# Optimization experiments

Measured on AMD Instinct MI355X. Metric: run time of the kernel, lower is better.

The kernel has to match this reference:

```python
import jax, jax.numpy as jnp
jax.config.update("jax_enable_x64", True)
import numpy as np

B, S, D, H = 2, 1024, 1024, 16
DEPTH = D // H  # 64


def setup_inputs() -> dict:
    key = jax.random.key(0)
    ks = jax.random.split(key, 12)
    inp = {
        "q": jax.random.normal(ks[0], (B, S, D), jnp.float32),
        "k": jax.random.normal(ks[1], (B, S, D), jnp.float32),
        "v": jax.random.normal(ks[2], (B, S - 1, D), jnp.float32),
        "e": jnp.zeros((1,), jnp.float32),  # unused by the layer
        "mask": jax.random.randint(ks[3], (B, S - 1, S - 1), 0, 2, jnp.int32),
        "Wq": jax.random.normal(ks[4], (D, D), jnp.float32) * 0.02,
        "bq": jnp.zeros((D,), jnp.float32),
        "Wk": jax.random.normal(ks[5], (D, D), jnp.float32) * 0.02,
        "bk": jnp.zeros((D,), jnp.float32),
        "Wv": jax.random.normal(ks[6], (D, D), jnp.float32) * 0.02,
        "bv": jnp.zeros((D,), jnp.float32),
        "Wo": jax.random.normal(ks[7], (D, D), jnp.float32) * 0.02,
        "bo": jnp.zeros((D,), jnp.float32),
    }
    return inp


def _split_heads(x, b):
    # [b, s, D] -> [b, H, s, DEPTH]
    return x.reshape(b, -1, H, DEPTH).transpose(0, 2, 1, 3)


def reference(q, k, v, e, mask, Wq, bq, Wk, bk, Wv, bv, Wo, bo):
    b = q.shape[0]
    qh = _split_heads(q @ Wq + bq, b)  # [b,H,S,dh]
    kh = _split_heads(k @ Wk + bk, b)  # [b,H,S,dh]
    vh = _split_heads(v @ Wv + bv, b)  # [b,H,S-1,dh]
    # QK^T then asymmetric offset slice [1:, :-1]
    scores = jnp.einsum("bhqd,bhkd->bhqk", qh, kh)[:, :, 1:, :-1]  # [b,H,S-1,S-1]
    inv_sqrt_dk = 1.0 / jnp.sqrt(jnp.float32(DEPTH))
    nl_qk = jax.nn.relu(scores * inv_sqrt_dk).astype(jnp.float64)
    nl_qk = nl_qk + mask[:, None, :, :].astype(jnp.float64) * (-1e9)
    att_weights = jax.nn.softmax(nl_qk, axis=-1)  # fp64, [b,H,S-1,S-1]
    out = jnp.einsum("bhqk,bhkd->bhqd", att_weights, vh.astype(jnp.float64))
    out = out.transpose(0, 2, 1, 3).reshape(b, -1, H * DEPTH)  # [b,S-1,D]
    output = out.astype(jnp.float32) @ Wo + bo
    return (output, att_weights)
```

## Files before the change

kernel.cpp:

```cpp
#include <hip/hip_runtime.h>
#include <math.h>

#define HN 16
#define SEQ 1024
#define DMODEL 1024
#define DH 64
#define SM1 1023

typedef float  f32x4  __attribute__((ext_vector_type(4)));
typedef __bf16 bf16x8 __attribute__((ext_vector_type(8)));

template<int MODE>
__global__ __launch_bounds__(256)
void gemm_mfma_kernel(const float* __restrict__ X, const float* __restrict__ W,
                      const float* __restrict__ bias, float* __restrict__ out32,
                      __bf16* __restrict__ outHi, __bf16* __restrict__ outLo,
                      int M, int rows)
{
    __shared__ __align__(16) __bf16 As[4096];
    __shared__ __align__(16) __bf16 Bs[4096];

    const int t  = threadIdx.x;
    const int w  = t >> 6, l = t & 63;
    const int lr = l & 15, ls = l >> 4;
    const int m0 = blockIdx.y * 64, n0 = blockIdx.x * 64;
    const int sr  = t >> 2;
    const int skq = t & 3;

    f32x4 acc[4];
#pragma unroll
    for (int ct = 0; ct < 4; ++ct) acc[ct] = f32x4{0.f, 0.f, 0.f, 0.f};

    const int ar   = w * 16 + lr;
    const int a_hi = ar * 128 + (((2 * ls    ) ^ (ar & 7)) << 4);
    const int a_lo = ar * 128 + (((2 * ls + 1) ^ (ar & 7)) << 4);
    const int st_hi = sr * 128 + (((2 * skq    ) ^ (sr & 7)) << 4);
    const int st_lo = sr * 128 + (((2 * skq + 1) ^ (sr & 7)) << 4);

    for (int k0 = 0; k0 < DMODEL; k0 += 32) {
        __syncthreads();
        {
            float xv[8];
            if (m0 + sr < M) {
                float4 v0 = *(const float4*)&X[(size_t)(m0 + sr) * DMODEL + k0 + skq * 8];
                float4 v1 = *(const float4*)&X[(size_t)(m0 + sr) * DMODEL + k0 + skq * 8 + 4];
                xv[0] = v0.x; xv[1] = v0.y; xv[2] = v0.z; xv[3] = v0.w;
                xv[4] = v1.x; xv[5] = v1.y; xv[6] = v1.z; xv[7] = v1.w;
            } else {
#pragma unroll
                for (int e = 0; e < 8; ++e) xv[e] = 0.f;
            }
            bf16x8 h8, l8;
#pragma unroll
            for (int e = 0; e < 8; ++e) {
                __bf16 hb = (__bf16)xv[e];
                h8[e] = hb;
                l8[e] = (__bf16)(xv[e] - (float)hb);
            }
            *(bf16x8*)((char*)As + st_hi) = h8;
            *(bf16x8*)((char*)As + st_lo) = l8;
        }
        {
            float wv[8];
#pragma unroll
            for (int e = 0; e < 8; ++e)
                wv[e] = W[(size_t)(k0 + skq * 8 + e) * DMODEL + n0 + sr];
            bf16x8 h8, l8;
#pragma unroll
            for (int e = 0; e < 8; ++e) {
                __bf16 hb = (__bf16)wv[e];
                h8[e] = hb;
                l8[e] = (__bf16)(wv[e] - (float)hb);
            }
            *(bf16x8*)((char*)Bs + st_hi) = h8;
            *(bf16x8*)((char*)Bs + st_lo) = l8;
        }
        __syncthreads();

        const bf16x8 ah = *(const bf16x8*)((const char*)As + a_hi);
        const bf16x8 al = *(const bf16x8*)((const char*)As + a_lo);
#pragma unroll
        for (int ct = 0; ct < 4; ++ct) {
            const int bc   = ct * 16 + lr;
            const int b_hi = bc * 128 + (((2 * ls    ) ^ (bc & 7)) << 4);
            const int b_lo = bc * 128 + (((2 * ls + 1) ^ (bc & 7)) << 4);
            const bf16x8 bh = *(const bf16x8*)((const char*)Bs + b_hi);
            const bf16x8 bl = *(const bf16x8*)((const char*)Bs + b_lo);
            acc[ct] = __builtin_amdgcn_mfma_f32_16x16x32_bf16(ah, bh, acc[ct], 0, 0, 0);
            acc[ct] = __builtin_amdgcn_mfma_f32_16x16x32_bf16(al, bh, acc[ct], 0, 0, 0);
            acc[ct] = __builtin_amdgcn_mfma_f32_16x16x32_bf16(ah, bl, acc[ct], 0, 0, 0);
        }
    }

#pragma unroll
    for (int ct = 0; ct < 4; ++ct) {
        const int n = n0 + ct * 16 + lr;
        const float bv = bias[n];
#pragma unroll
        for (int j = 0; j < 4; ++j) {
            const int m = m0 + w * 16 + ls * 4 + j;
            if (m >= M) continue;
            const float val = acc[ct][j] + bv;
            if (MODE == 1) {
                out32[(size_t)m * DMODEL + n] = val;
            } else {
                const int bb = m / rows, s = m - bb * rows;
                const __bf16 hb = (__bf16)val;
                const __bf16 lb = (__bf16)(val - (float)hb);
                size_t idx;
                if (MODE == 0)
                    idx = (((size_t)(bb * HN + (n >> 6)) * SEQ + s) << 6) + (n & 63);
                else
                    idx = (((size_t)(bb * HN + (n >> 6)) * DH + (n & 63)) << 10) + s;
                outHi[idx] = hb; outLo[idx] = lb;
            }
        }
    }
}

__global__ __launch_bounds__(256)
void mask_pack_kernel(const int* __restrict__ mask, unsigned int* __restrict__ mb)
{
    const int row = blockIdx.x * 4 + (threadIdx.x >> 6);
    const int l   = threadIdx.x & 63;
    if (row >= 2 * SM1) return;
    const int* mrow = mask + (size_t)row * SM1;
    unsigned int* out = mb + (size_t)row * 32;
#pragma unroll
    for (int i = 0; i < 16; ++i) {
        const int c = i * 64 + l;
        const bool mv = (c < SM1) && (mrow[c] != 0);
        unsigned long long bal = __ballot(mv);
        if (l == 0) {
            out[i * 2]     = (unsigned int)bal;
            out[i * 2 + 1] = (unsigned int)(bal >> 32);
        }
    }
}

__global__ __launch_bounds__(512, 4)
void attn_fused_kernel(const __bf16* __restrict__ qhi, const __bf16* __restrict__ qlo,
                       const __bf16* __restrict__ khi, const __bf16* __restrict__ klo,
                       const __bf16* __restrict__ vthi, const __bf16* __restrict__ vtlo,
                       const unsigned int* __restrict__ mbG,
                       float* __restrict__ att, float* __restrict__ ctx)
{
    __shared__ __align__(16) char QE[64 * 528];
    __shared__ __align__(16) char KV[32768];
    __shared__ unsigned int mbitsT[32][64];
    __shared__ float invs[64];
    __shared__ float partial[64][2];

    const int id  = blockIdx.x;
    const int xcd = id & 7, slot = id >> 3;
    const int bh  = xcd + 8 * (slot >> 4);
    const int b   = bh >> 4, h = bh & 15;
    const int q0  = (slot & 15) * 64;

    const int t = threadIdx.x, w = t >> 6, l = t & 63;
    const int lr = l & 15, ls = l >> 4;
    const int g = w & 3, p = w >> 2;

#pragma unroll
    for (int it = 0; it < 2; ++it) {
        const int idq = t + it * 512;
        const int r = idq >> 4, cw = idq & 15;
        const int plane = cw >> 3, s = cw & 7;
        int qrow = q0 + r + 1; if (qrow > 1023) qrow = 1023;
        const __bf16* src = plane ? qlo : qhi;
        bf16x8 vv = *(const bf16x8*)&src[((size_t)bh * SEQ + qrow) * DH + s * 8];
        *(bf16x8*)(QE + r * 256 + ((cw ^ (r & 15)) << 4)) = vv;
    }
#pragma unroll
    for (int it = 0; it < 4; ++it) {
        const int idm = t + it * 512;
        const int cw = idm & 31, r = idm >> 5;
        const int rr = q0 + r;
        mbitsT[cw][r] = (rr < SM1) ? mbG[((size_t)b * SM1 + rr) * 32 + cw] : 0u;
    }
    __syncthreads();

    const int ar = g * 16 + lr;
    const bf16x8 a0h = *(const bf16x8*)(QE + ar * 256 + (((ls     ) ^ lr) << 4));
    const bf16x8 a1h = *(const bf16x8*)(QE + ar * 256 + ((( 4 + ls) ^ lr) << 4));
    const bf16x8 a0l = *(const bf16x8*)(QE + ar * 256 + ((( 8 + ls) ^ lr) << 4));
    const bf16x8 a1l = *(const bf16x8*)(QE + ar * 256 + (((12 + ls) ^ lr) << 4));
    __syncthreads();

    float rsum[4] = {0.f, 0.f, 0.f, 0.f};
    for (int kt = 0; kt < 8; ++kt) {
        const int c0 = kt * 128;
        __syncthreads();
#pragma unroll
        for (int it = 0; it < 4; ++it) {
            const int idk = t + it * 512;
            const int r = idk >> 4, cw = idk & 15;
            const int plane = cw >> 3, s = cw & 7;
            int krow = c0 + r; if (krow > 1023) krow = 1023;
            const __bf16* src = plane ? klo : khi;
            bf16x8 vv = *(const bf16x8*)&src[((size_t)bh * SEQ + krow) * DH + s * 8];
            *(bf16x8*)(KV + r * 256 + ((cw ^ (r & 15)) << 4)) = vv;
        }
        __syncthreads();

#pragma unroll
        for (int i = 0; i < 4; ++i) {
            const int ct = p * 4 + i;
            const int kr = ct * 16 + lr;
            const bf16x8 b0h = *(const bf16x8*)(KV + kr * 256 + (((ls     ) ^ lr) << 4));
            const bf16x8 b1h = *(const bf16x8*)(KV + kr * 256 + ((( 4 + ls) ^ lr) << 4));
            const bf16x8 b0l = *(const bf16x8*)(KV + kr * 256 + ((( 8 + ls) ^ lr) << 4));
            const bf16x8 b1l = *(const bf16x8*)(KV + kr * 256 + (((12 + ls) ^ lr) << 4));

            f32x4 acc = {0.f, 0.f, 0.f, 0.f};
            __builtin_amdgcn_s_setprio(1);
            acc = __builtin_amdgcn_mfma_f32_16x16x32_bf16(a0h, b0h, acc, 0, 0, 0);
            acc = __builtin_amdgcn_mfma_f32_16x16x32_bf16(a0l, b0h, acc, 0, 0, 0);
            acc = __builtin_amdgcn_mfma_f32_16x16x32_bf16(a0h, b0l, acc, 0, 0, 0);
            acc = __builtin_amdgcn_mfma_f32_16x16x32_bf16(a1h, b1h, acc, 0, 0, 0);
            acc = __builtin_amdgcn_mfma_f32_16x16x32_bf16(a1l, b1h, acc, 0, 0, 0);
            acc = __builtin_amdgcn_mfma_f32_16x16x32_bf16(a1h, b1l, acc, 0, 0, 0);
            __builtin_amdgcn_s_setprio(0);

            const int c = c0 + ct * 16 + lr;
            const int wmi = kt * 4 + (ct >> 1);
#pragma unroll
            for (int j = 0; j < 4; ++j) {
                const int r = q0 + g * 16 + ls * 4 + j;
                if (r < SM1 && c < SM1) {
                    float sc = fmaxf(acc[j] * 0.125f, 0.f);
                    const unsigned int wm = mbitsT[wmi][g * 16 + ls * 4 + j];
                    if ((wm >> ((ct & 1) * 16 + lr)) & 1u) sc = -1e9f;
                    rsum[j] += __expf(sc);
                }
            }
        }
    }
#pragma unroll
    for (int j = 0; j < 4; ++j) {
        rsum[j] += __shfl_xor(rsum[j], 1, 64);
        rsum[j] += __shfl_xor(rsum[j], 2, 64);
        rsum[j] += __shfl_xor(rsum[j], 4, 64);
        rsum[j] += __shfl_xor(rsum[j], 8, 64);
    }
    if (lr == 0) {
#pragma unroll
        for (int j = 0; j < 4; ++j)
            partial[g * 16 + ls * 4 + j][p] = rsum[j];
    }
    __syncthreads();
    if (t < 64) {
        const float s = partial[t][0] + partial[t][1];
        invs[t] = (q0 + t < SM1) ? 1.0f / s : 0.f;
    }
    __syncthreads();
    float inv4[4];
#pragma unroll
    for (int j = 0; j < 4; ++j) inv4[j] = invs[g * 16 + ls * 4 + j];

    float* E = (float*)QE;
    f32x4 oacc[4];
#pragma unroll
    for (int ct = 0; ct < 4; ++ct) oacc[ct] = f32x4{0.f, 0.f, 0.f, 0.f};

    for (int kt = 0; kt < 8; ++kt) {
        const int c0 = kt * 128;
        __syncthreads();
#pragma unroll
        for (int it = 0; it < 4; ++it) {
            const int idk = t + it * 512;
            const int r = idk >> 4, cw = idk & 15;
            const int plane = cw >> 3, s = cw & 7;
            int krow = c0 + r; if (krow > 1023) krow = 1023;
            const __bf16* src = plane ? klo : khi;
            bf16x8 vv = *(const bf16x8*)&src[((size_t)bh * SEQ + krow) * DH + s * 8];
            *(bf16x8*)(KV + r * 256 + ((cw ^ (r & 15)) << 4)) = vv;
        }
        __syncthreads();

#pragma unroll
        for (int i = 0; i < 4; ++i) {
            const int ct = p * 4 + i;
            const int kr = ct * 16 + lr;
            const bf16x8 b0h = *(const bf16x8*)(KV + kr * 256 + (((ls     ) ^ lr) << 4));
            const bf16x8 b1h = *(const bf16x8*)(KV + kr * 256 + ((( 4 + ls) ^ lr) << 4));
            const bf16x8 b0l = *(const bf16x8*)(KV + kr * 256 + ((( 8 + ls) ^ lr) << 4));
            const bf16x8 b1l = *(const bf16x8*)(KV + kr * 256 + (((12 + ls) ^ lr) << 4));

            f32x4 acc = {0.f, 0.f, 0.f, 0.f};
            __builtin_amdgcn_s_setprio(1);
            acc = __builtin_amdgcn_mfma_f32_16x16x32_bf16(a0h, b0h, acc, 0, 0, 0);
            acc = __builtin_amdgcn_mfma_f32_16x16x32_bf16(a0l, b0h, acc, 0, 0, 0);
            acc = __builtin_amdgcn_mfma_f32_16x16x32_bf16(a0h, b0l, acc, 0, 0, 0);
            acc = __builtin_amdgcn_mfma_f32_16x16x32_bf16(a1h, b1h, acc, 0, 0, 0);
            acc = __builtin_amdgcn_mfma_f32_16x16x32_bf16(a1l, b1h, acc, 0, 0, 0);
            acc = __builtin_amdgcn_mfma_f32_16x16x32_bf16(a1h, b1l, acc, 0, 0, 0);
            __builtin_amdgcn_s_setprio(0);

            const int c = c0 + ct * 16 + lr;
            const int wmi = kt * 4 + (ct >> 1);
#pragma unroll
            for (int j = 0; j < 4; ++j) {
                const int r = q0 + g * 16 + ls * 4 + j;
                float v = 0.f;
                if (r < SM1 && c < SM1) {
                    float sc = fmaxf(acc[j] * 0.125f, 0.f);
                    const unsigned int wm = mbitsT[wmi][g * 16 + ls * 4 + j];
                    if ((wm >> ((ct & 1) * 16 + lr)) & 1u) sc = -1e9f;
                    v = __expf(sc) * inv4[j];
                }
                E[(g * 16 + ls * 4 + j) * 132 + ct * 16 + lr] = v;
            }
        }
        __syncthreads();

#pragma unroll
        for (int it = 0; it < 4; ++it) {
            const int idv = t + it * 512;
            const int dr = idv >> 5, cw = idv & 31;
            const int plane = cw >> 4, s8 = cw & 15;
            const __bf16* src = plane ? vtlo : vthi;
            bf16x8 vv = *(const bf16x8*)&src[(((size_t)bh * DH + dr) << 10) + c0 + s8 * 8];
            *(bf16x8*)(KV + dr * 512 + ((cw ^ (dr & 31)) << 4)) = vv;
        }
#pragma unroll
        for (int it = 0; it < 4; ++it) {
            const int idw = t + it * 512;
            const int r = idw >> 5, q4 = idw & 31;
            const int rr = q0 + r, cc = c0 + q4 * 4;
            if (rr < SM1) {
                f32x4 vv = *(const f32x4*)&E[r * 132 + q4 * 4];
                float* dst = &att[((size_t)bh * SM1 + rr) * SM1 + cc];
                if (cc + 4 <= SM1) {
                    __builtin_nontemporal_store(vv, (f32x4*)dst);
                } else {
                    if (cc + 0 < SM1) dst[0] = vv.x;
                    if (cc + 1 < SM1) dst[1] = vv.y;
                    if (cc + 2 < SM1) dst[2] = vv.z;
                }
            }
        }
        __syncthreads();

#pragma unroll
        for (int m = 0; m < 2; ++m) {
            const int ks = p * 2 + m;
            const int pr = g * 16 + lr;
            const f32x4 p0 = *(const f32x4*)&E[pr * 132 + ks * 32 + ls * 8];
            const f32x4 p1 = *(const f32x4*)&E[pr * 132 + ks * 32 + ls * 8 + 4];
            float pf[8] = {p0.x, p0.y, p0.z, p0.w, p1.x, p1.y, p1.z, p1.w};
            bf16x8 ph, pl;
#pragma unroll
            for (int e = 0; e < 8; ++e) {
                const __bf16 hb = (__bf16)pf[e];
                ph[e] = hb;
                pl[e] = (__bf16)(pf[e] - (float)hb);
            }
#pragma unroll
            for (int ct = 0; ct < 4; ++ct) {
                const int vr = ct * 16 + lr;
                const int hslot = ((ks * 4 + ls) ^ (vr & 31));
                const int lslot = ((16 + ks * 4 + ls) ^ (vr & 31));
                const bf16x8 vh = *(const bf16x8*)(KV + vr * 512 + (hslot << 4));
                const bf16x8 vl = *(const bf16x8*)(KV + vr * 512 + (lslot << 4));
                __builtin_amdgcn_s_setprio(1);
                oacc[ct] = __builtin_amdgcn_mfma_f32_16x16x32_bf16(ph, vh, oacc[ct], 0, 0, 0);
                oacc[ct] = __builtin_amdgcn_mfma_f32_16x16x32_bf16(pl, vh, oacc[ct], 0, 0, 0);
                oacc[ct] = __builtin_amdgcn_mfma_f32_16x16x32_bf16(ph, vl, oacc[ct], 0, 0, 0);
                __builtin_amdgcn_s_setprio(0);
            }
        }
    }

    __syncthreads();
    float* red = (float*)QE;
    if (p == 1) {
#pragma unroll
        for (int ct = 0; ct < 4; ++ct)
#pragma unroll
            for (int j = 0; j < 4; ++j)
                red[(g * 16 + ls * 4 + j) * 68 + ct * 16 + lr] = oacc[ct][j];
    }
    __syncthreads();
    if (p == 0) {
#pragma unroll
        for (int ct = 0; ct < 4; ++ct)
#pragma unroll
            for (int j = 0; j < 4; ++j) {
                const int r = q0 + g * 16 + ls * 4 + j;
                if (r < SM1)
                    ctx[((size_t)b * SM1 + r) * DMODEL + h * DH + ct * 16 + lr] =
                        oacc[ct][j] + red[(g * 16 + ls * 4 + j) * 68 + ct * 16 + lr];
            }
    }
}

extern "C" void kernel_launch(void* const* d_in, const int* in_sizes, int n_in,
                              void* d_out, int out_size, void* d_ws, size_t ws_size,
                              hipStream_t stream) {
    const float* q    = (const float*)d_in[0];
    const float* k    = (const float*)d_in[1];
    const float* v    = (const float*)d_in[2];
    const int*   mask = (const int*)  d_in[4];
    const float* Wq   = (const float*)d_in[5];
    const float* bq   = (const float*)d_in[6];
    const float* Wk   = (const float*)d_in[7];
    const float* bk   = (const float*)d_in[8];
    const float* Wv   = (const float*)d_in[9];
    const float* bv   = (const float*)d_in[10];
    const float* Wo   = (const float*)d_in[11];
    const float* bo   = (const float*)d_in[12];

    float* out0 = (float*)d_out;
    float* att  = out0 + (size_t)2 * SM1 * DMODEL;

    const size_t NQ  = (size_t)2 * HN * SEQ * DH;
    const size_t NVT = (size_t)2 * HN * DH * 1024;
    __bf16* ws16 = (__bf16*)d_ws;
    __bf16* qhi  = ws16;
    __bf16* qlo  = qhi + NQ;
    __bf16* khi  = qlo + NQ;
    __bf16* klo  = khi + NQ;
    __bf16* vthi = klo + NQ;
    __bf16* vtlo = vthi + NVT;
    float*  ctx  = (float*)(vtlo + NVT);
    unsigned int* mbG = (unsigned int*)(ctx + (size_t)2 * SM1 * DMODEL);

    (void)hipMemsetAsync(vthi, 0, 2 * NVT * sizeof(__bf16), stream);

    mask_pack_kernel<<<dim3(512), 256, 0, stream>>>(mask, mbG);

    gemm_mfma_kernel<0><<<dim3(16, 32), 256, 0, stream>>>(q, Wq, bq, nullptr, qhi, qlo, 2 * SEQ, SEQ);
    gemm_mfma_kernel<0><<<dim3(16, 32), 256, 0, stream>>>(k, Wk, bk, nullptr, khi, klo, 2 * SEQ, SEQ);
    gemm_mfma_kernel<2><<<dim3(16, 32), 256, 0, stream>>>(v, Wv, bv, nullptr, vthi, vtlo, 2 * SM1, SM1);

    attn_fused_kernel<<<dim3(512), 512, 0, stream>>>(qhi, qlo, khi, klo, vthi, vtlo, mbG, att, ctx);

    gemm_mfma_kernel<1><<<dim3(16, 32), 256, 0, stream>>>(ctx, Wo, bo, out0, nullptr, nullptr, 2 * SM1, SM1);
}
```

Baseline: 265.5 us.

## Prefetch GEMM and attention tiles into registers to overlap global loads

The projection GEMM moves to double-buffered shared memory, with the next K-slice loaded into registers during the MFMA work on the current one, so there is one barrier per iteration instead of two. In the attention kernel, the K and V tiles are register-prefetched one step ahead in both passes, and the V load is issued while the score tile is still being computed. The goal is to hide global-memory latency behind MFMA work, at the cost of more registers and more shared memory in the GEMM, which may reduce occupancy.

Measured after the change: 276.3 us. 1.04x slower.

```diff
diff --git a/kernel.cpp b/kernel.cpp
--- a/kernel.cpp
+++ b/kernel.cpp
@@ -17,8 +17,8 @@
                       __bf16* __restrict__ outHi, __bf16* __restrict__ outLo,
                       int M, int rows)
 {
-    __shared__ __align__(16) __bf16 As[4096];
-    __shared__ __align__(16) __bf16 Bs[4096];
+    __shared__ __align__(16) __bf16 As[2][4096];
+    __shared__ __align__(16) __bf16 Bs[2][4096];
 
     const int t  = threadIdx.x;
     const int w  = t >> 6, l = t & 63;
@@ -26,6 +26,7 @@
     const int m0 = blockIdx.y * 64, n0 = blockIdx.x * 64;
     const int sr  = t >> 2;
     const int skq = t & 3;
+    const bool arow_ok = (m0 + sr < M);
 
     f32x4 acc[4];
 #pragma unroll
@@ -37,59 +38,61 @@
     const int st_hi = sr * 128 + (((2 * skq    ) ^ (sr & 7)) << 4);
     const int st_lo = sr * 128 + (((2 * skq + 1) ^ (sr & 7)) << 4);
 
-    for (int k0 = 0; k0 < DMODEL; k0 += 32) {
-        __syncthreads();
-        {
-            float xv[8];
-            if (m0 + sr < M) {
-                float4 v0 = *(const float4*)&X[(size_t)(m0 + sr) * DMODEL + k0 + skq * 8];
-                float4 v1 = *(const float4*)&X[(size_t)(m0 + sr) * DMODEL + k0 + skq * 8 + 4];
-                xv[0] = v0.x; xv[1] = v0.y; xv[2] = v0.z; xv[3] = v0.w;
-                xv[4] = v1.x; xv[5] = v1.y; xv[6] = v1.z; xv[7] = v1.w;
-            } else {
-#pragma unroll
-                for (int e = 0; e < 8; ++e) xv[e] = 0.f;
-            }
-            bf16x8 h8, l8;
-#pragma unroll
-            for (int e = 0; e < 8; ++e) {
-                __bf16 hb = (__bf16)xv[e];
-                h8[e] = hb;
-                l8[e] = (__bf16)(xv[e] - (float)hb);
-            }
-            *(bf16x8*)((char*)As + st_hi) = h8;
-            *(bf16x8*)((char*)As + st_lo) = l8;
-        }
-        {
-            float wv[8];
-#pragma unroll
-            for (int e = 0; e < 8; ++e)
-                wv[e] = W[(size_t)(k0 + skq * 8 + e) * DMODEL + n0 + sr];
-            bf16x8 h8, l8;
-#pragma unroll
-            for (int e = 0; e < 8; ++e) {
-                __bf16 hb = (__bf16)wv[e];
-                h8[e] = hb;
-                l8[e] = (__bf16)(wv[e] - (float)hb);
-            }
-            *(bf16x8*)((char*)Bs + st_hi) = h8;
-            *(bf16x8*)((char*)Bs + st_lo) = l8;
-        }
-        __syncthreads();
-
-        const bf16x8 ah = *(const bf16x8*)((const char*)As + a_hi);
-        const bf16x8 al = *(const bf16x8*)((const char*)As + a_lo);
+    float4 xv0, xv1;
+    float  wv[8];
+
+    auto LOADT = [&](int k0) {
+        if (arow_ok) {
+            xv0 = *(const float4*)&X[(size_t)(m0 + sr) * DMODEL + k0 + skq * 8];
+            xv1 = *(const float4*)&X[(size_t)(m0 + sr) * DMODEL + k0 + skq * 8 + 4];
+        } else {
+            xv0 = float4{0.f, 0.f, 0.f, 0.f};
+            xv1 = float4{0.f, 0.f, 0.f, 0.f};
+        }
+#pragma unroll
+        for (int e = 0; e < 8; ++e)
+            wv[e] = W[(size_t)(k0 + skq * 8 + e) * DMODEL + n0 + sr];
+    };
+    auto WRITET = [&](int buf) {
+        float xa[8] = {xv0.x, xv0.y, xv0.z, xv0.w, xv1.x, xv1.y, xv1.z, xv1.w};
+        bf16x8 ah8, al8, bh8, bl8;
+#pragma unroll
+        for (int e = 0; e < 8; ++e) {
+            __bf16 hb = (__bf16)xa[e];
+            ah8[e] = hb;
+            al8[e] = (__bf16)(xa[e] - (float)hb);
+            __bf16 wb = (__bf16)wv[e];
+            bh8[e] = wb;
+            bl8[e] = (__bf16)(wv[e] - (float)wb);
+        }
+        *(bf16x8*)((char*)As[buf] + st_hi) = ah8;
+        *(bf16x8*)((char*)As[buf] + st_lo) = al8;
+        *(bf16x8*)((char*)Bs[buf] + st_hi) = bh8;
+        *(bf16x8*)((char*)Bs[buf] + st_lo) = bl8;
+    };
+
+    LOADT(0);
+    WRITET(0);
+
+    for (int ks = 0; ks < 32; ++ks) {
+        const int cur = ks & 1;
+        if (ks < 31) LOADT((ks + 1) * 32);
+        __syncthreads();
+
+        const bf16x8 ah = *(const bf16x8*)((const char*)As[cur] + a_hi);
+        const bf16x8 al = *(const bf16x8*)((const char*)As[cur] + a_lo);
 #pragma unroll
         for (int ct = 0; ct < 4; ++ct) {
             const int bc   = ct * 16 + lr;
             const int b_hi = bc * 128 + (((2 * ls    ) ^ (bc & 7)) << 4);
             const int b_lo = bc * 128 + (((2 * ls + 1) ^ (bc & 7)) << 4);
-            const bf16x8 bh = *(const bf16x8*)((const char*)Bs + b_hi);
-            const bf16x8 bl = *(const bf16x8*)((const char*)Bs + b_lo);
+            const bf16x8 bh = *(const bf16x8*)((const char*)Bs[cur] + b_hi);
+            const bf16x8 bl = *(const bf16x8*)((const char*)Bs[cur] + b_lo);
             acc[ct] = __builtin_amdgcn_mfma_f32_16x16x32_bf16(ah, bh, acc[ct], 0, 0, 0);
             acc[ct] = __builtin_amdgcn_mfma_f32_16x16x32_bf16(al, bh, acc[ct], 0, 0, 0);
             acc[ct] = __builtin_amdgcn_mfma_f32_16x16x32_bf16(ah, bl, acc[ct], 0, 0, 0);
         }
+        if (ks < 31) WRITET(cur ^ 1);
     }
 
 #pragma unroll
@@ -161,6 +164,34 @@
     const int lr = l & 15, ls = l >> 4;
     const int g = w & 3, p = w >> 2;
 
+    int k_roff[4], k_doff[4], k_soff[4];
+#pragma unroll
+    for (int it = 0; it < 4; ++it) {
+        const int idk = t + it * 512;
+        const int r = idk >> 4, cw = idk & 15;
+        k_roff[it] = r;
+        k_soff[it] = (cw & 7) * 8 + ((cw >> 3) ? 1 : 0) * 0;
+        k_doff[it] = r * 256 + ((cw ^ (r & 15)) << 4);
+    }
+    int k_plane[4];
+#pragma unroll
+    for (int it = 0; it < 4; ++it) {
+        const int idk = t + it * 512;
+        k_plane[it] = (idk & 15) >> 3;
+    }
+    int v_droff[4], v_soff[4], v_doff[4], v_plane[4];
+#pragma unroll
+    for (int it = 0; it < 4; ++it) {
+        const int idv = t + it * 512;
+        const int dr = idv >> 5, cw = idv & 31;
+        v_droff[it] = dr;
+        v_plane[it] = cw >> 4;
+        v_soff[it]  = (cw & 15) * 8;
+        v_doff[it]  = dr * 512 + ((cw ^ (dr & 31)) << 4);
+    }
+
+    bf16x8 kr[4], vr[4];
+
 #pragma unroll
     for (int it = 0; it < 2; ++it) {
         const int idq = t + it * 512;
@@ -187,30 +218,52 @@
     const bf16x8 a1l = *(const bf16x8*)(QE + ar * 256 + (((12 + ls) ^ lr) << 4));
     __syncthreads();
 
+#define LOADK(c0_)                                                              \
+    {                                                                           \
+        _Pragma("unroll")                                                       \
+        for (int it = 0; it < 4; ++it) {                                        \
+            int krow = (c0_) + k_roff[it]; if (krow > 1023) krow = 1023;        \
+            const __bf16* src = k_plane[it] ? klo : khi;                        \
+            kr[it] = *(const bf16x8*)&src[((size_t)bh * SEQ + krow) * DH + k_soff[it]]; \
+        }                                                                       \
+    }
+#define WRITEK()                                                                \
+    {                                                                           \
+        _Pragma("unroll")                                                       \
+        for (int it = 0; it < 4; ++it)                                          \
+            *(bf16x8*)(KV + k_doff[it]) = kr[it];                               \
+    }
+#define LOADV(c0_)                                                              \
+    {                                                                           \
+        _Pragma("unroll")                                                       \
+        for (int it = 0; it < 4; ++it) {                                        \
+            const __bf16* src = v_plane[it] ? vtlo : vthi;                      \
+            vr[it] = *(const bf16x8*)&src[(((size_t)bh * DH + v_droff[it]) << 10) + (c0_) + v_soff[it]]; \
+        }                                                                       \
+    }
+#define WRITEV()                                                                \
+    {                                                                           \
+        _Pragma("unroll")                                                       \
+        for (int it = 0; it < 4; ++it)                                          \
+            *(bf16x8*)(KV + v_doff[it]) = vr[it];                               \
+    }
+
     float rsum[4] = {0.f, 0.f, 0.f, 0.f};
+    LOADK(0);
+    WRITEK();
     for (int kt = 0; kt < 8; ++kt) {
         const int c0 = kt * 128;
-        __syncthreads();
-#pragma unroll
-        for (int it = 0; it < 4; ++it) {
-            const int idk = t + it * 512;
-            const int r = idk >> 4, cw = idk & 15;
-            const int plane = cw >> 3, s = cw & 7;
-            int krow = c0 + r; if (krow > 1023) krow = 1023;
-            const __bf16* src = plane ? klo : khi;
-            bf16x8 vv = *(const bf16x8*)&src[((size_t)bh * SEQ + krow) * DH + s * 8];
-            *(bf16x8*)(KV + r * 256 + ((cw ^ (r & 15)) << 4)) = vv;
-        }
+        if (kt < 7) LOADK(c0 + 128);
         __syncthreads();
 
 #pragma unroll
         for (int i = 0; i < 4; ++i) {
             const int ct = p * 4 + i;
-            const int kr = ct * 16 + lr;
-            const bf16x8 b0h = *(const bf16x8*)(KV + kr * 256 + (((ls     ) ^ lr) << 4));
-            const bf16x8 b1h = *(const bf16x8*)(KV + kr * 256 + ((( 4 + ls) ^ lr) << 4));
-            const bf16x8 b0l = *(const bf16x8*)(KV + kr * 256 + ((( 8 + ls) ^ lr) << 4));
-            const bf16x8 b1l = *(const bf16x8*)(KV + kr * 256 + (((12 + ls) ^ lr) << 4));
+            const int kr16 = ct * 16 + lr;
+            const bf16x8 b0h = *(const bf16x8*)(KV + kr16 * 256 + (((ls     ) ^ lr) << 4));
+            const bf16x8 b1h = *(const bf16x8*)(KV + kr16 * 256 + ((( 4 + ls) ^ lr) << 4));
+            const bf16x8 b0l = *(const bf16x8*)(KV + kr16 * 256 + ((( 8 + ls) ^ lr) << 4));
+            const bf16x8 b1l = *(const bf16x8*)(KV + kr16 * 256 + (((12 + ls) ^ lr) << 4));
 
             f32x4 acc = {0.f, 0.f, 0.f, 0.f};
             __builtin_amdgcn_s_setprio(1);
@@ -235,7 +288,12 @@
                 }
             }
         }
-    }
+        __syncthreads();
+        if (kt < 7) WRITEK();
+    }
+
+    LOADK(0);
+
 #pragma unroll
     for (int j = 0; j < 4; ++j) {
         rsum[j] += __shfl_xor(rsum[j], 1, 64);
@@ -266,26 +324,18 @@
     for (int kt = 0; kt < 8; ++kt) {
         const int c0 = kt * 128;
         __syncthreads();
-#pragma unroll
-        for (int it = 0; it < 4; ++it) {
-            const int idk = t + it * 512;
-            const int r = idk >> 4, cw = idk & 15;
-            const int plane = cw >> 3, s = cw & 7;
-            int krow = c0 + r; if (krow > 1023) krow = 1023;
-            const __bf16* src = plane ? klo : khi;
-            bf16x8 vv = *(const bf16x8*)&src[((size_t)bh * SEQ + krow) * DH + s * 8];
-            *(bf16x8*)(KV + r * 256 + ((cw ^ (r & 15)) << 4)) = vv;
-        }
+        WRITEK();
+        LOADV(c0);
         __syncthreads();
 
 #pragma unroll
         for (int i = 0; i < 4; ++i) {
             const int ct = p * 4 + i;
-            const int kr = ct * 16 + lr;
-            const bf16x8 b0h = *(const bf16x8*)(KV + kr * 256 + (((ls     ) ^ lr) << 4));
-            const bf16x8 b1h = *(const bf16x8*)(KV + kr * 256 + ((( 4 + ls) ^ lr) << 4));
-            const bf16x8 b0l = *(const bf16x8*)(KV + kr * 256 + ((( 8 + ls) ^ lr) << 4));
-            const bf16x8 b1l = *(const bf16x8*)(KV + kr * 256 + (((12 + ls) ^ lr) << 4));
+            const int kr16 = ct * 16 + lr;
+            const bf16x8 b0h = *(const bf16x8*)(KV + kr16 * 256 + (((ls     ) ^ lr) << 4));
+            const bf16x8 b1h = *(const bf16x8*)(KV + kr16 * 256 + ((( 4 + ls) ^ lr) << 4));
+            const bf16x8 b0l = *(const bf16x8*)(KV + kr16 * 256 + ((( 8 + ls) ^ lr) << 4));
+            const bf16x8 b1l = *(const bf16x8*)(KV + kr16 * 256 + (((12 + ls) ^ lr) << 4));
 
             f32x4 acc = {0.f, 0.f, 0.f, 0.f};
             __builtin_amdgcn_s_setprio(1);
@@ -312,17 +362,10 @@
                 E[(g * 16 + ls * 4 + j) * 132 + ct * 16 + lr] = v;
             }
         }
-        __syncthreads();
-
-#pragma unroll
-        for (int it = 0; it < 4; ++it) {
-            const int idv = t + it * 512;
-            const int dr = idv >> 5, cw = idv & 31;
-            const int plane = cw >> 4, s8 = cw & 15;
-            const __bf16* src = plane ? vtlo : vthi;
-            bf16x8 vv = *(const bf16x8*)&src[(((size_t)bh * DH + dr) << 10) + c0 + s8 * 8];
-            *(bf16x8*)(KV + dr * 512 + ((cw ^ (dr & 31)) << 4)) = vv;
-        }
+        if (kt < 7) LOADK(c0 + 128);
+        __syncthreads();
+
+        WRITEV();
 #pragma unroll
         for (int it = 0; it < 4; ++it) {
             const int idw = t + it * 512;
@@ -358,11 +401,11 @@
             }
 #pragma unroll
             for (int ct = 0; ct < 4; ++ct) {
-                const int vr = ct * 16 + lr;
-                const int hslot = ((ks * 4 + ls) ^ (vr & 31));
-                const int lslot = ((16 + ks * 4 + ls) ^ (vr & 31));
-                const bf16x8 vh = *(const bf16x8*)(KV + vr * 512 + (hslot << 4));
-                const bf16x8 vl = *(const bf16x8*)(KV + vr * 512 + (lslot << 4));
+                const int vr16 = ct * 16 + lr;
+                const int hslot = ((ks * 4 + ls) ^ (vr16 & 31));
+                const int lslot = ((16 + ks * 4 + ls) ^ (vr16 & 31));
+                const bf16x8 vh = *(const bf16x8*)(KV + vr16 * 512 + (hslot << 4));
+                const bf16x8 vl = *(const bf16x8*)(KV + vr16 * 512 + (lslot << 4));
                 __builtin_amdgcn_s_setprio(1);
                 oacc[ct] = __builtin_amdgcn_mfma_f32_16x16x32_bf16(ph, vh, oacc[ct], 0, 0, 0);
                 oacc[ct] = __builtin_amdgcn_mfma_f32_16x16x32_bf16(pl, vh, oacc[ct], 0, 0, 0);
@@ -393,6 +436,10 @@
                         oacc[ct][j] + red[(g * 16 + ls * 4 + j) * 68 + ct * 16 + lr];
             }
     }
+#undef LOADK
+#undef WRITEK
+#undef LOADV
+#undef WRITEV
 }
 
 extern "C" void kernel_launch(void* const* d_in, const int* in_sizes, int n_in,
```
